# Kernel optimization log

Hardware: AMD Instinct MI355X
Metric: run time of the kernel (lower is better)

## Reference

```python
import jax, jax.numpy as jnp
import numpy as np

SHIFT = 1  # fixed shift_direction (original picks +-1 randomly at init)


def setup_inputs() -> dict:
    key = jax.random.key(0)
    kx, kw = jax.random.split(key)
    x = jax.random.normal(kx, (128, 256, 28, 28), dtype=jnp.float32)
    W = jax.random.normal(kw, (32, 3, 4, 3, 8), dtype=jnp.float32)
    return {"x": x, "W": W}


def reference(x, W):
    # (128,256,28,28) -> (128,2,128,28,28) -> sum over dim 1 -> (128,128,28,28)
    t = x.reshape(128, 2, 128, 28, 28).sum(axis=1)
    # split channels into 32 groups of 4: (n, i=32, m=4, h=28, w=28)
    t = t.reshape(128, 32, 4, 28, 28)
    # first unfold: kernel (3,1), pad (1,0) over the i=32 axis -> neighbor stack j in {-1,0,+1}
    tp = jnp.pad(t, ((0, 0), (1, 1), (0, 0), (0, 0), (0, 0)))
    t3 = jnp.stack([tp[:, 0:32], tp[:, 1:33], tp[:, 2:34]], axis=1)  # (n, j3, i32, m, h, w)
    # cyclic shift along w
    t3 = jnp.roll(t3, SHIFT, axis=5)
    # second unfold: kernel (3,1), pad (1,0) over the w axis -> neighbor stack kw in {-1,0,+1}
    tp2 = jnp.pad(t3, ((0, 0), (0, 0), (0, 0), (0, 0), (0, 0), (1, 1)))
    t3 = jnp.stack([tp2[..., 0:28], tp2[..., 1:29], tp2[..., 2:30]], axis=5)  # (n, j3, i32, m, h, kw, w)
    # contraction: einsum labels match torch 'njimpol,jimlk->njpok' after its permute.
    # Our t3 dims (n, i_e=3, j_e=32, m=4, p=h, l=kw, o=w); W dims (j=32, i=3, m=4, l=3, k=8)
    out = jnp.einsum('nijmplo,jimlk->njpok', t3, W)  # (128, 32, 28, 28, 8)
    out = out.transpose(0, 2, 3, 1, 4).reshape(128, 28, 28, 256)
    out = jnp.roll(out, SHIFT, axis=1)
    return out.transpose(0, 3, 1, 2)  # (128, 256, 28, 28)
```

## Files before the change

kernel.cpp:

```cpp
#include <hip/hip_runtime.h>

typedef float __attribute__((ext_vector_type(4))) f32x4;
typedef unsigned int u32;
typedef u32 __attribute__((ext_vector_type(4))) u32x4;


__device__ __forceinline__ u32 pack2bf(float lo, float hi) {
    u32 a = __float_as_uint(lo), b = __float_as_uint(hi);
    a = (a + 0x7FFFu + ((a >> 16) & 1u)) >> 16;
    b = (b + 0x7FFFu + ((b >> 16) & 1u)) >> 16;
    return a | (b << 16);
}

__device__ __forceinline__ float dot2bf(u32 t2, u32 w2, float acc) {
    asm("v_dot2_f32_bf16 %0, %1, %2, %0" : "+v"(acc) : "v"(t2), "v"(w2));
    return acc;
}

__global__ __launch_bounds__(512, 8) void fused_shift_conv(
    const float* __restrict__ x, const float* __restrict__ Wt, float* __restrict__ out)
{
    __shared__ __align__(16) u32 L[7680];

    const int tid = threadIdx.x;
    const int blk = blockIdx.x;
    const int n   = blk / 14;
    const int b2  = blk - n * 14;
    const int h0  = b2 * 2;

    const float* xn = x + (size_t)n * 200704;

    #pragma unroll
    for (int it = 0; it < 2; ++it) {
        const int f = tid + it * 512;
        if (f < 896) {
            const int p     = f / 14;
            const int rem14 = f - p * 14;
            const int row   = rem14 / 7;
            const int q     = rem14 - row * 7;
            int hs = h0 - 1 + row;
            hs = hs < 0 ? 27 : hs;
            const float* b0 = xn + (2 * p) * 784 + hs * 28 + q * 4;
            const f32x4 l0 = *(const f32x4*)b0;
            const f32x4 l1 = *(const f32x4*)(b0 + 784);
            const f32x4 u0 = *(const f32x4*)(b0 + 100352);
            const f32x4 u1 = *(const f32x4*)(b0 + 784 + 100352);
            const f32x4 s0 = l0 + u0, s1 = l1 + u1;
            u32x4 wv;
            #pragma unroll
            for (int e = 0; e < 4; ++e) wv[e] = pack2bf(s0[e], s1[e]);
            const int sw = (p >> 1) & 7;
            *(u32x4*)&L[row * 2048 + p * 32 + ((q ^ sw) << 2)] = wv;
        }
    }

    const int t  = tid & 255;
    const int s_ = tid >> 8;
    const int j = t >> 3, k = t & 7;
    u32 w2[3][2][3];
    {
        const float* wp = Wt + j * 288 + k;
        #pragma unroll
        for (int a = 0; a < 3; ++a)
            #pragma unroll
            for (int m2 = 0; m2 < 2; ++m2)
                #pragma unroll
                for (int bb = 0; bb < 3; ++bb)
                    w2[a][m2][bb] = pack2bf(wp[a*96 + (2*m2  )*24 + bb*8],
                                            wp[a*96 + (2*m2+1)*24 + bb*8]);
    }
    if (j == 0) {
        #pragma unroll
        for (int m2 = 0; m2 < 2; ++m2)
            #pragma unroll
            for (int bb = 0; bb < 3; ++bb) w2[0][m2][bb] = 0u;
    }
    if (j == 31) {
        #pragma unroll
        for (int m2 = 0; m2 < 2; ++m2)
            #pragma unroll
            for (int bb = 0; bb < 3; ++bb) w2[2][m2][bb] = 0u;
    }

    int o_lds[4], o_glb[4];
    #pragma unroll
    for (int it = 0; it < 4; ++it) {
        const int fo  = tid + it * 512;
        const int chl = fo / 14;
        const int rem = fo - chl * 14;
        o_lds[it] = chl * 60 + rem * 4;
        o_glb[it] = chl * 784 + h0 * 28 + rem * 4;
    }

    __syncthreads();

    const u32* Bs = L + s_ * 2048;
    float acc[28];
    #pragma unroll
    for (int w = 0; w < 28; ++w) acc[w] = 0.f;

    #pragma unroll
    for (int a = 0; a < 3; ++a) {
        int g = j + a - 1;
        g = g < 0 ? 0 : (g > 31 ? 31 : g);
        const int s = g & 7;
        #pragma unroll
        for (int m2 = 0; m2 < 2; ++m2) {
            const int rowd = (g * 2 + m2) * 32;
            const u32 t2 = w2[a][m2][2], t1 = w2[a][m2][1], t0 = w2[a][m2][0];
            #pragma unroll
            for (int qb = 0; qb < 7; ++qb) {
                const u32x4 v = *(const u32x4*)&Bs[rowd + ((qb ^ s) << 2)];
                #pragma unroll
                for (int e = 0; e < 4; ++e) {
                    const int wp_ = qb * 4 + e;
                    if (wp_ != 27) acc[wp_] = dot2bf(v[e], t2, acc[wp_]);
                    acc[(wp_ + 1) % 28] = dot2bf(v[e], t1, acc[(wp_ + 1) % 28]);
                    if (wp_ != 26) acc[(wp_ + 2) % 28] = dot2bf(v[e], t0, acc[(wp_ + 2) % 28]);
                }
            }
        }
    }

    float* Lf = (float*)L;
    float* outn = out + (size_t)n * 200704;
    #pragma unroll
    for (int c = 0; c < 2; ++c) {
        __syncthreads();
        if ((j >> 4) == c) {
            const int oc = (j & 15) * 8 + k;
            float* dst = Lf + oc * 60 + s_ * 28;
            #pragma unroll
            for (int qq = 0; qq < 7; ++qq) {
                f32x4 o;
                o.x = acc[qq * 4 + 0];
                o.y = acc[qq * 4 + 1];
                o.z = acc[qq * 4 + 2];
                o.w = acc[qq * 4 + 3];
                *(f32x4*)(dst + qq * 4) = o;
            }
        }
        __syncthreads();
        float* outc = outn + (size_t)c * 128 * 784;
        #pragma unroll
        for (int it = 0; it < 4; ++it) {
            if (tid + it * 512 < 1792) {
                const f32x4 v = *(const f32x4*)(Lf + o_lds[it]);
                *(f32x4*)(outc + o_glb[it]) = v;
            }
        }
    }
}

extern "C" void kernel_launch(void* const* d_in, const int* in_sizes, int n_in,
                              void* d_out, int out_size, void* d_ws, size_t ws_size,
                              hipStream_t stream) {
    const float* x  = (const float*)d_in[0];
    const float* Wt = (const float*)d_in[1];
    float* out      = (float*)d_out;

    const int nbatch = in_sizes[0] / 200704;
    fused_shift_conv<<<nbatch * 14, 512, 0, stream>>>(x, Wt, out);
}
```

Measured before the change: 50.12 us.

## Split each block's output channels in half with halo-loaded input groups

Each block now covers 16 of the 32 channel groups for a pair of output rows, so the grid doubles to 28 blocks per batch and each block has 256 threads. Each half stages 18 channel groups (16 plus one halo group on each side, zero-filled at the edges) into a smaller LDS buffer, and the output write-back is restricted to the 128 channels the half owns. The aim is more, smaller blocks for better occupancy and load balance across CUs. The cost is that each half re-reads and re-sums its two halo groups, so about an eighth more input traffic.

Measured after the change: 50.37 us. No clear change (+0.5%).

```diff
diff --git a/kernel.cpp b/kernel.cpp
--- a/kernel.cpp
+++ b/kernel.cpp
@@ -17,46 +17,57 @@
     return acc;
 }
 
-__global__ __launch_bounds__(512, 8) void fused_shift_conv(
+__global__ __launch_bounds__(256, 8) void fused_shift_conv(
     const float* __restrict__ x, const float* __restrict__ Wt, float* __restrict__ out)
 {
-    __shared__ __align__(16) u32 L[7680];
+    __shared__ __align__(16) u32 L[3840];
 
-    const int tid = threadIdx.x;
-    const int blk = blockIdx.x;
-    const int n   = blk / 14;
-    const int b2  = blk - n * 14;
-    const int h0  = b2 * 2;
+    const int tid  = threadIdx.x;
+    const int blk  = blockIdx.x;
+    const int half = blk & 1;
+    const int rest = blk >> 1;
+    const int n    = rest / 14;
+    const int b2   = rest - n * 14;
+    const int h0   = b2 * 2;
+    const int J0   = half * 16;
 
     const float* xn = x + (size_t)n * 200704;
 
     #pragma unroll
     for (int it = 0; it < 2; ++it) {
-        const int f = tid + it * 512;
-        if (f < 896) {
-            const int p     = f / 14;
-            const int rem14 = f - p * 14;
-            const int row   = rem14 / 7;
-            const int q     = rem14 - row * 7;
+        const int f = tid + it * 256;
+        if (f < 504) {
+            const int pl  = f / 14;
+            const int rem = f - pl * 14;
+            const int row = rem / 7;
+            const int q   = rem - row * 7;
+            const int gl  = pl >> 1;
+            const int mp  = pl & 1;
+            const int g   = J0 - 1 + gl;
             int hs = h0 - 1 + row;
             hs = hs < 0 ? 27 : hs;
-            const float* b0 = xn + (2 * p) * 784 + hs * 28 + q * 4;
-            const f32x4 l0 = *(const f32x4*)b0;
-            const f32x4 l1 = *(const f32x4*)(b0 + 784);
-            const f32x4 u0 = *(const f32x4*)(b0 + 100352);
-            const f32x4 u1 = *(const f32x4*)(b0 + 784 + 100352);
-            const f32x4 s0 = l0 + u0, s1 = l1 + u1;
-            u32x4 wv;
-            #pragma unroll
-            for (int e = 0; e < 4; ++e) wv[e] = pack2bf(s0[e], s1[e]);
-            const int sw = (p >> 1) & 7;
-            *(u32x4*)&L[row * 2048 + p * 32 + ((q ^ sw) << 2)] = wv;
+            u32x4 wv = {0u, 0u, 0u, 0u};
+            if (g >= 0 && g <= 31) {
+                const int ch0 = g * 4 + mp * 2;
+                const float* b0 = xn + ch0 * 784 + hs * 28 + q * 4;
+                const f32x4 l0 = *(const f32x4*)b0;
+                const f32x4 l1 = *(const f32x4*)(b0 + 784);
+                const f32x4 u0 = *(const f32x4*)(b0 + 100352);
+                const f32x4 u1 = *(const f32x4*)(b0 + 784 + 100352);
+                const f32x4 s0 = l0 + u0, s1 = l1 + u1;
+                #pragma unroll
+                for (int e = 0; e < 4; ++e) wv[e] = pack2bf(s0[e], s1[e]);
+            }
+            const int sw = gl & 7;
+            *(u32x4*)&L[row * 1152 + pl * 32 + ((q ^ sw) << 2)] = wv;
         }
     }
 
-    const int t  = tid & 255;
-    const int s_ = tid >> 8;
-    const int j = t >> 3, k = t & 7;
+    const int tloc = tid & 127;
+    const int s_   = tid >> 7;
+    const int jl   = tloc >> 3;
+    const int j    = J0 + jl;
+    const int k    = tloc & 7;
     u32 w2[3][2][3];
     {
         const float* wp = Wt + j * 288 + k;
@@ -82,31 +93,28 @@
             for (int bb = 0; bb < 3; ++bb) w2[2][m2][bb] = 0u;
     }
 
-    int o_lds[4], o_glb[4];
+    int rb_c[4], rb_r[4];
     #pragma unroll
     for (int it = 0; it < 4; ++it) {
-        const int fo  = tid + it * 512;
-        const int chl = fo / 14;
-        const int rem = fo - chl * 14;
-        o_lds[it] = chl * 60 + rem * 4;
-        o_glb[it] = chl * 784 + h0 * 28 + rem * 4;
+        const int fo = tid + it * 256;
+        rb_c[it] = fo / 14;
+        rb_r[it] = fo - rb_c[it] * 14;
     }
 
     __syncthreads();
 
-    const u32* Bs = L + s_ * 2048;
+    const u32* Bs = L + s_ * 1152;
     float acc[28];
     #pragma unroll
     for (int w = 0; w < 28; ++w) acc[w] = 0.f;
 
     #pragma unroll
     for (int a = 0; a < 3; ++a) {
-        int g = j + a - 1;
-        g = g < 0 ? 0 : (g > 31 ? 31 : g);
-        const int s = g & 7;
+        const int gl = jl + a;
+        const int s  = gl & 7;
         #pragma unroll
         for (int m2 = 0; m2 < 2; ++m2) {
-            const int rowd = (g * 2 + m2) * 32;
+            const int rowd = (gl * 2 + m2) * 32;
             const u32 t2 = w2[a][m2][2], t1 = w2[a][m2][1], t0 = w2[a][m2][0];
             #pragma unroll
             for (int qb = 0; qb < 7; ++qb) {
@@ -123,13 +131,12 @@
     }
 
     float* Lf = (float*)L;
-    float* outn = out + (size_t)n * 200704;
+    float* outb = out + (size_t)n * 200704 + (size_t)(J0 * 8) * 784 + h0 * 28;
     #pragma unroll
     for (int c = 0; c < 2; ++c) {
         __syncthreads();
-        if ((j >> 4) == c) {
-            const int oc = (j & 15) * 8 + k;
-            float* dst = Lf + oc * 60 + s_ * 28;
+        if ((tloc >> 6) == c) {
+            float* dst = Lf + (tloc & 63) * 60 + s_ * 28;
             #pragma unroll
             for (int qq = 0; qq < 7; ++qq) {
                 f32x4 o;
@@ -141,12 +148,12 @@
             }
         }
         __syncthreads();
-        float* outc = outn + (size_t)c * 128 * 784;
+        float* outc = outb + (size_t)(c * 64) * 784;
         #pragma unroll
         for (int it = 0; it < 4; ++it) {
-            if (tid + it * 512 < 1792) {
-                const f32x4 v = *(const f32x4*)(Lf + o_lds[it]);
-                *(f32x4*)(outc + o_glb[it]) = v;
+            if (tid + it * 256 < 896) {
+                const f32x4 v = *(const f32x4*)(Lf + rb_c[it] * 60 + rb_r[it] * 4);
+                *(f32x4*)(outc + (size_t)rb_c[it] * 784 + rb_r[it] * 4) = v;
             }
         }
     }
@@ -160,5 +167,5 @@
     float* out      = (float*)d_out;
 
     const int nbatch = in_sizes[0] / 200704;
-    fused_shift_conv<<<nbatch * 14, 512, 0, stream>>>(x, Wt, out);
+    fused_shift_conv<<<nbatch * 28, 256, 0, stream>>>(x, Wt, out);
 }
```
